# Performance work log

Measured on AMD Instinct MI355X. Metric: run time of the kernel, lower is better.

## Reference

```python
import jax, jax.numpy as jnp
import numpy as np

ALPHA = 0.2  # leaky relu slope
NEG_BIG = -9000000000000000.0


def setup_inputs() -> dict:
    key = jax.random.key(0)
    k1, k2, k3, k4 = jax.random.split(key, 4)
    B, N, Fin, Fout = 8, 2048, 256, 256
    h = jax.random.normal(k1, (B, N, Fin), dtype=jnp.float32)
    adj = jax.random.randint(k2, (B, N, N), 0, 2, dtype=jnp.int32)
    # xavier_uniform with gain=1.414
    gain = 1.414
    limW = gain * np.sqrt(6.0 / (Fin + Fout))
    W = jax.random.uniform(k3, (Fin, Fout), dtype=jnp.float32, minval=-limW, maxval=limW)
    lima = gain * np.sqrt(6.0 / (2 * Fout + 1))
    a = jax.random.uniform(k4, (2 * Fout, 1), dtype=jnp.float32, minval=-lima, maxval=lima)
    return {"h": h, "adj": adj, "W": W, "a": a}


def reference(h, adj, W, a):
    # Wh: [B, N, F]
    Wh = jnp.matmul(h, W)
    Fout = W.shape[1]
    a1 = a[:Fout, 0]   # scores for source node i (repeat_interleave side)
    a2 = a[Fout:, 0]   # scores for target node j (repeat side)
    # e[b,i,j] = leakyrelu(Wh[b,i]@a1 + Wh[b,j]@a2)  -- decomposed, no O(N^2 * 2F) tensor
    s1 = jnp.einsum('bnf,f->bn', Wh, a1)  # [B, N]
    s2 = jnp.einsum('bnf,f->bn', Wh, a2)  # [B, N]
    e = jax.nn.leaky_relu(s1[:, :, None] + s2[:, None, :], negative_slope=ALPHA)
    masked = jnp.where(adj > 0, e, jnp.full_like(e, NEG_BIG))
    attention = jax.nn.softmax(masked, axis=2)  # dropout=0 (eval mode)
    h_prime = jnp.matmul(attention, Wh)  # [B, N, F]
    return jax.nn.elu(h_prime)
```

## Files before the change

### kernel.cpp

```cpp
#include <hip/hip_runtime.h>

typedef __attribute__((ext_vector_type(8))) short bhalf8;
typedef __attribute__((ext_vector_type(4))) float floatx4;

#define ALPHA_LR 0.2f

__device__ __forceinline__ unsigned short f2bf(float f) {
  union { float f; unsigned int u; } v; v.f = f;
  unsigned int r = v.u + 0x7fffu + ((v.u >> 16) & 1u);
  return (unsigned short)(r >> 16);
}
__device__ __forceinline__ float bf2f(unsigned short u) {
  union { unsigned int u; float f; } v; v.u = ((unsigned int)u) << 16;
  return v.f;
}
__device__ __forceinline__ void gld16(const void* g, void* l) {
  __builtin_amdgcn_global_load_lds((const __attribute__((address_space(1))) unsigned int*)g,
                                   (__attribute__((address_space(3))) unsigned int*)l,
                                   16, 0, 0);
}

__global__ void k0w_split(const float* __restrict__ W,
                          unsigned short* __restrict__ WThi,
                          unsigned short* __restrict__ WTlo,
                          unsigned int* __restrict__ s2maxEnc) {
  __shared__ float s[16][17];
  const int tx = threadIdx.x, ty = threadIdx.y;
  if (blockIdx.x == 0 && blockIdx.y == 0 && ty == 0 && tx < 8) s2maxEnc[tx] = 0u;
  const int n0 = blockIdx.x * 16, k0 = blockIdx.y * 16;
  s[ty][tx] = W[(k0 + ty) * 256 + n0 + tx];
  __syncthreads();
  float v = s[tx][ty];
  const int k = k0 + tx, n = n0 + ty;
  unsigned short hi = f2bf(v);
  unsigned short lo = f2bf(v - bf2f(hi));
  const int idx = (k >> 5) * 8192 + n * 32 + (k & 31);
  WThi[idx] = hi;
  WTlo[idx] = lo;
}

__global__ __launch_bounds__(512, 2) void k1_mfma(const float* __restrict__ h,
                                                  const unsigned short* __restrict__ Bhi_g,
                                                  const unsigned short* __restrict__ Blo_g,
                                                  const float* __restrict__ a_g,
                                                  unsigned short* __restrict__ WhPack,
                                                  float* __restrict__ s1,
                                                  float* __restrict__ s2,
                                                  unsigned int* __restrict__ s2maxEnc) {
  __shared__ unsigned short Ah[64 * 264], Al[64 * 264];
  __shared__ unsigned short Bh[2][8192], Bl[2][8192];
  __shared__ float s1red[64], s2red[64];
  const int t = threadIdx.x;
  const long r0 = (long)blockIdx.x * 64;
  const int wave = t >> 6, lane = t & 63;

  if (t < 64) { s1red[t] = 0.f; s2red[t] = 0.f; }

#pragma unroll
  for (int rep = 0; rep < 2; rep++) {
    const int off = wave * 1024 + rep * 512;
    gld16(Bhi_g + off + lane * 8, &Bh[0][off]);
    gld16(Blo_g + off + lane * 8, &Bl[0][off]);
  }

#pragma unroll
  for (int q = 0; q < 8; q++) {
    int idx = q * 512 + t;
    int row = idx >> 6, c4 = idx & 63;
    float4 x = *(const float4*)(h + (r0 + row) * 256 + c4 * 4);
    float xs[4] = {x.x, x.y, x.z, x.w};
    unsigned short hs[4], ls[4];
#pragma unroll
    for (int qq = 0; qq < 4; qq++) {
      hs[qq] = f2bf(xs[qq]);
      ls[qq] = f2bf(xs[qq] - bf2f(hs[qq]));
    }
    *(ushort4*)&Ah[row * 264 + c4 * 4] = (ushort4){hs[0], hs[1], hs[2], hs[3]};
    *(ushort4*)&Al[row * 264 + c4 * 4] = (ushort4){ls[0], ls[1], ls[2], ls[3]};
  }
  __syncthreads();

  const int wm = wave >> 2, wn = wave & 3;
  const int lhi = lane >> 4, llo = lane & 15;

  floatx4 acc[2][4];
#pragma unroll
  for (int mt = 0; mt < 2; mt++)
#pragma unroll
    for (int nt = 0; nt < 4; nt++) acc[mt][nt] = (floatx4){0.f, 0.f, 0.f, 0.f};

  for (int ks = 0; ks < 8; ks++) {
    const int cur = ks & 1, nxt = cur ^ 1, ksn = (ks + 1) & 7;
#pragma unroll
    for (int rep = 0; rep < 2; rep++) {
      const int off = wave * 1024 + rep * 512;
      gld16(Bhi_g + ksn * 8192 + off + lane * 8, &Bh[nxt][off]);
      gld16(Blo_g + ksn * 8192 + off + lane * 8, &Bl[nxt][off]);
    }

    const int k0 = ks * 32;
    bhalf8 ah[2], al[2], bh[4], bl[4];
#pragma unroll
    for (int mt = 0; mt < 2; mt++) {
      int ro = (wm * 32 + mt * 16 + llo) * 264 + k0 + lhi * 8;
      ah[mt] = *(const bhalf8*)&Ah[ro];
      al[mt] = *(const bhalf8*)&Al[ro];
    }
#pragma unroll
    for (int nt = 0; nt < 4; nt++) {
      int ro = (wn * 64 + nt * 16 + llo) * 32 + lhi * 8;
      bh[nt] = *(const bhalf8*)&Bh[cur][ro];
      bl[nt] = *(const bhalf8*)&Bl[cur][ro];
    }
#pragma unroll
    for (int mt = 0; mt < 2; mt++)
#pragma unroll
      for (int nt = 0; nt < 4; nt++) {
        acc[mt][nt] = __builtin_amdgcn_mfma_f32_16x16x32_bf16(ah[mt], bh[nt], acc[mt][nt], 0, 0, 0);
        acc[mt][nt] = __builtin_amdgcn_mfma_f32_16x16x32_bf16(ah[mt], bl[nt], acc[mt][nt], 0, 0, 0);
        acc[mt][nt] = __builtin_amdgcn_mfma_f32_16x16x32_bf16(al[mt], bh[nt], acc[mt][nt], 0, 0, 0);
      }
    __syncthreads();
  }

  float a1v[4], a2v[4];
#pragma unroll
  for (int nt = 0; nt < 4; nt++) {
    int f = wn * 64 + nt * 16 + llo;
    a1v[nt] = a_g[f];
    a2v[nt] = a_g[256 + f];
  }

  const int b = (int)(r0 >> 11);
  const int jt_base = (int)((r0 & 2047) >> 5);

#pragma unroll
  for (int mt = 0; mt < 2; mt++) {
    float p1[4], p2[4];
#pragma unroll
    for (int reg = 0; reg < 4; reg++) {
      p1[reg] = acc[mt][0][reg] * a1v[0] + acc[mt][1][reg] * a1v[1] +
                acc[mt][2][reg] * a1v[2] + acc[mt][3][reg] * a1v[3];
      p2[reg] = acc[mt][0][reg] * a2v[0] + acc[mt][1][reg] * a2v[1] +
                acc[mt][2][reg] * a2v[2] + acc[mt][3][reg] * a2v[3];
    }
#pragma unroll
    for (int off = 1; off < 16; off <<= 1) {
#pragma unroll
      for (int reg = 0; reg < 4; reg++) {
        p1[reg] += __shfl_xor(p1[reg], off);
        p2[reg] += __shfl_xor(p2[reg], off);
      }
    }
    if (llo == 0) {
#pragma unroll
      for (int reg = 0; reg < 4; reg++) {
        int il = wm * 32 + mt * 16 + lhi * 4 + reg;
        atomicAdd(&s1red[il], p1[reg]);
        atomicAdd(&s2red[il], p2[reg]);
      }
    }
#pragma unroll
    for (int nt = 0; nt < 4; nt++) {
      int f = wn * 64 + nt * 16 + llo;
      int jt = jt_base + wm;
      ushort4 pk = (ushort4){f2bf(acc[mt][nt][0]), f2bf(acc[mt][nt][1]),
                             f2bf(acc[mt][nt][2]), f2bf(acc[mt][nt][3])};
      *(ushort4*)&WhPack[((long)((b * 64 + jt) * 256 + f)) * 32 + mt * 16 + lhi * 4] = pk;
    }
  }

  __syncthreads();
  if (t < 64) {
    s1[r0 + t] = s1red[t];
    s2[r0 + t] = s2red[t];
    float v = s2red[t];
#pragma unroll
    for (int o = 32; o; o >>= 1) v = fmaxf(v, __shfl_xor(v, o));
    if (t == 0) {
      unsigned int u = __float_as_uint(v);
      unsigned int key = (u & 0x80000000u) ? ~u : (u | 0x80000000u);
      atomicMax(s2maxEnc + b, key);
    }
  }
}

__global__ __launch_bounds__(512, 2) void k3_attn(const unsigned short* __restrict__ WhPack,
                                                  const int* __restrict__ adj,
                                                  const float* __restrict__ s1g,
                                                  const float* __restrict__ s2g,
                                                  const unsigned int* __restrict__ s2maxEnc,
                                                  float* __restrict__ out) {
  const int t = threadIdx.x;
  const int lin = blockIdx.x;
  const int b = lin & 7;
  const int ig = lin >> 3;
  const int wave = t >> 6, lane = t & 63;
  const int rg = wave >> 2, fg = wave & 3;
  const int i0 = ig * 64 + rg * 32;
  const long gr0 = (long)b * 2048 + i0;
  const int llo = lane & 15, lhi = lane >> 4;

  const unsigned int ek = s2maxEnc[b];
  const float s2max = (ek & 0x80000000u) ? __uint_as_float(ek & 0x7fffffffu)
                                         : __uint_as_float(~ek);
  float s1i[2], Mi[2];
#pragma unroll
  for (int mt = 0; mt < 2; mt++) {
    s1i[mt] = s1g[gr0 + mt * 16 + llo];
    float xm = s1i[mt] + s2max;
    Mi[mt] = fmaxf(xm, ALPHA_LR * xm);
  }

  const float* s2p = s2g + (long)b * 2048 + lhi * 8;
  const int* ap0 = adj + (gr0 + llo) * 2048 + lhi * 8;
  const int* ap1 = ap0 + 16 * 2048;
  const unsigned short* wb =
      WhPack + (long)b * 524288 + (long)((fg * 64 + llo) * 32 + lhi * 8);

  int4 cA0 = *(const int4*)ap0, cB0 = *(const int4*)(ap0 + 4);
  int4 cA1 = *(const int4*)ap1, cB1 = *(const int4*)(ap1 + 4);
  int4 nA0 = *(const int4*)(ap0 + 32), nB0 = *(const int4*)(ap0 + 36);
  int4 nA1 = *(const int4*)(ap1 + 32), nB1 = *(const int4*)(ap1 + 36);
  float4 s2A = *(const float4*)s2p;
  float4 s2B = *(const float4*)(s2p + 4);
  bhalf8 bF[4];
#pragma unroll
  for (int nt = 0; nt < 4; nt++) bF[nt] = *(const bhalf8*)(wb + nt * 512);

  floatx4 acc[2][4];
#pragma unroll
  for (int mt = 0; mt < 2; mt++)
#pragma unroll
    for (int nt = 0; nt < 4; nt++) acc[mt][nt] = (floatx4){0.f, 0.f, 0.f, 0.f};
  float ls0 = 0.f, ls1 = 0.f;

#pragma unroll 2
  for (int jt = 0; jt < 64; jt++) {
    const int jn = (jt < 63) ? jt + 1 : 63;
    const int j2 = (jt < 62) ? jt + 2 : 63;

    bhalf8 bFn[4];
#pragma unroll
    for (int nt = 0; nt < 4; nt++)
      bFn[nt] = *(const bhalf8*)(wb + (long)jn * 8192 + nt * 512);
    float4 s2nA = *(const float4*)(s2p + jn * 32);
    float4 s2nB = *(const float4*)(s2p + jn * 32 + 4);
    int4 mA0 = *(const int4*)(ap0 + j2 * 32), mB0 = *(const int4*)(ap0 + j2 * 32 + 4);
    int4 mA1 = *(const int4*)(ap1 + j2 * 32), mB1 = *(const int4*)(ap1 + j2 * 32 + 4);

    __builtin_amdgcn_sched_barrier(0);

    bhalf8 pa[2];
#pragma unroll
    for (int mt = 0; mt < 2; mt++) {
      const float s1v = s1i[mt], miv = Mi[mt];
      const int4 aA = mt ? cA1 : cA0;
      const int4 aB = mt ? cB1 : cB0;
      float xs[8] = {s2A.x, s2A.y, s2A.z, s2A.w, s2B.x, s2B.y, s2B.z, s2B.w};
      int am[8] = {aA.x, aA.y, aA.z, aA.w, aB.x, aB.y, aB.z, aB.w};
      float e[8];
      float lsm = 0.f;
#pragma unroll
      for (int q = 0; q < 8; q++) {
        float x = s1v + xs[q];
        float lk = fmaxf(x, ALPHA_LR * x);
        float ee = __expf(lk - miv);
        ee = (am[q] > 0) ? ee : 0.f;
        lsm += ee;
        e[q] = ee;
      }
      if (mt) ls1 += lsm; else ls0 += lsm;
      union { unsigned int u[4]; bhalf8 v; } pk;
#pragma unroll
      for (int q = 0; q < 4; q++)
        asm("v_cvt_pk_bf16_f32 %0, %1, %2" : "=v"(pk.u[q]) : "v"(e[2 * q]), "v"(e[2 * q + 1]));
      pa[mt] = pk.v;
    }

#pragma unroll
    for (int mt = 0; mt < 2; mt++)
#pragma unroll
      for (int nt = 0; nt < 4; nt++)
        acc[mt][nt] = __builtin_amdgcn_mfma_f32_16x16x32_bf16(mt ? pa[1] : pa[0],
                                                              bF[nt], acc[mt][nt], 0, 0, 0);

    cA0 = nA0; cB0 = nB0; cA1 = nA1; cB1 = nB1;
    nA0 = mA0; nB0 = mB0; nA1 = mA1; nB1 = mB1;
    s2A = s2nA; s2B = s2nB;
#pragma unroll
    for (int nt = 0; nt < 4; nt++) bF[nt] = bFn[nt];
  }

  ls0 += __shfl_xor(ls0, 16); ls0 += __shfl_xor(ls0, 32);
  ls1 += __shfl_xor(ls1, 16); ls1 += __shfl_xor(ls1, 32);
  float inv0 = 1.f / fmaxf(ls0, 1e-35f);
  float inv1 = 1.f / fmaxf(ls1, 1e-35f);

#pragma unroll
  for (int mt = 0; mt < 2; mt++) {
#pragma unroll
    for (int reg = 0; reg < 4; reg++) {
      const int rloc = lhi * 4 + reg;
      float iv = __shfl(mt ? inv1 : inv0, rloc);
      const long orow = (gr0 + mt * 16 + rloc) * 256 + fg * 64 + llo;
#pragma unroll
      for (int nt = 0; nt < 4; nt++) {
        float v = acc[mt][nt][reg] * iv;
        v = v > 0.f ? v : expm1f(v);
        out[orow + nt * 16] = v;
      }
    }
  }
}

extern "C" void kernel_launch(void* const* d_in, const int* in_sizes, int n_in,
                              void* d_out, int out_size, void* d_ws, size_t ws_size,
                              hipStream_t stream) {
  const float* h = (const float*)d_in[0];
  const int* adj = (const int*)d_in[1];
  const float* W = (const float*)d_in[2];
  const float* a = (const float*)d_in[3];
  float* out = (float*)d_out;

  char* ws = (char*)d_ws;
  unsigned short* WhPack = (unsigned short*)ws;
  unsigned short* WThi = (unsigned short*)(ws + 8388608);
  unsigned short* WTlo = (unsigned short*)(ws + 8519680);
  float* s1 = (float*)(ws + 8650752);
  float* s2 = (float*)(ws + 8716288);
  unsigned int* s2maxEnc = (unsigned int*)(ws + 8781824);

  hipLaunchKernelGGL(k0w_split, dim3(16, 16), dim3(16, 16), 0, stream, W, WThi, WTlo, s2maxEnc);
  hipLaunchKernelGGL(k1_mfma, dim3(256), dim3(512), 0, stream, h, WThi, WTlo, a,
                     WhPack, s1, s2, s2maxEnc);
  hipLaunchKernelGGL(k3_attn, dim3(256), dim3(512), 0, stream, WhPack, adj,
                     s1, s2, s2maxEnc, out);
}
```

Before: 288.8 us.

## Pack adjacency into bitmask in a pre-pass and read bits in attention kernel

Adds a streaming kernel that reads the int32 adjacency matrix once with coalesced loads and uses wave ballots to write a 1-bit-per-edge mask. The attention kernel then loads one 32-bit mask word per row per tile instead of eight int32 values per lane, and drops its two-tile-ahead adjacency prefetch. The aim is to shrink the attention kernel's memory traffic and register pressure, and to remove redundant adjacency reads across the feature-group waves. The cost is an extra kernel launch and a separate full pass over the 128MB adjacency tensor.

```diff
diff --git a/kernel.cpp b/kernel.cpp
--- a/kernel.cpp
+++ b/kernel.cpp
@@ -39,6 +39,31 @@
   WTlo[idx] = lo;
 }
 
+__global__ __launch_bounds__(256) void k2_pack(const int* __restrict__ adj,
+                                               unsigned long long* __restrict__ mask) {
+  const int wave = threadIdx.x >> 6, lane = threadIdx.x & 63;
+  const long wid = (long)blockIdx.x * 4 + wave;
+  const long u0 = wid * 64;
+  const int* base = adj + u0 * 64 + lane;
+#pragma unroll
+  for (int it = 0; it < 64; it += 4) {
+    int v0 = base[(it + 0) * 64];
+    int v1 = base[(it + 1) * 64];
+    int v2 = base[(it + 2) * 64];
+    int v3 = base[(it + 3) * 64];
+    unsigned long long m0 = __ballot(v0 > 0);
+    unsigned long long m1 = __ballot(v1 > 0);
+    unsigned long long m2 = __ballot(v2 > 0);
+    unsigned long long m3 = __ballot(v3 > 0);
+    if (lane == 0) {
+      mask[u0 + it + 0] = m0;
+      mask[u0 + it + 1] = m1;
+      mask[u0 + it + 2] = m2;
+      mask[u0 + it + 3] = m3;
+    }
+  }
+}
+
 __global__ __launch_bounds__(512, 2) void k1_mfma(const float* __restrict__ h,
                                                   const unsigned short* __restrict__ Bhi_g,
                                                   const unsigned short* __restrict__ Blo_g,
@@ -186,7 +211,7 @@
 }
 
 __global__ __launch_bounds__(512, 2) void k3_attn(const unsigned short* __restrict__ WhPack,
-                                                  const int* __restrict__ adj,
+                                                  const unsigned int* __restrict__ mask32,
                                                   const float* __restrict__ s1g,
                                                   const float* __restrict__ s2g,
                                                   const unsigned int* __restrict__ s2maxEnc,
@@ -200,6 +225,7 @@
   const int i0 = ig * 64 + rg * 32;
   const long gr0 = (long)b * 2048 + i0;
   const int llo = lane & 15, lhi = lane >> 4;
+  const int sh = lhi * 8;
 
   const unsigned int ek = s2maxEnc[b];
   const float s2max = (ek & 0x80000000u) ? __uint_as_float(ek & 0x7fffffffu)
@@ -213,15 +239,12 @@
   }
 
   const float* s2p = s2g + (long)b * 2048 + lhi * 8;
-  const int* ap0 = adj + (gr0 + llo) * 2048 + lhi * 8;
-  const int* ap1 = ap0 + 16 * 2048;
+  const unsigned int* mp0 = mask32 + (gr0 + llo) * 64;
+  const unsigned int* mp1 = mp0 + 16 * 64;
   const unsigned short* wb =
       WhPack + (long)b * 524288 + (long)((fg * 64 + llo) * 32 + lhi * 8);
 
-  int4 cA0 = *(const int4*)ap0, cB0 = *(const int4*)(ap0 + 4);
-  int4 cA1 = *(const int4*)ap1, cB1 = *(const int4*)(ap1 + 4);
-  int4 nA0 = *(const int4*)(ap0 + 32), nB0 = *(const int4*)(ap0 + 36);
-  int4 nA1 = *(const int4*)(ap1 + 32), nB1 = *(const int4*)(ap1 + 36);
+  unsigned int cm0 = mp0[0], cm1 = mp1[0];
   float4 s2A = *(const float4*)s2p;
   float4 s2B = *(const float4*)(s2p + 4);
   bhalf8 bF[4];
@@ -238,7 +261,6 @@
 #pragma unroll 2
   for (int jt = 0; jt < 64; jt++) {
     const int jn = (jt < 63) ? jt + 1 : 63;
-    const int j2 = (jt < 62) ? jt + 2 : 63;
 
     bhalf8 bFn[4];
 #pragma unroll
@@ -246,8 +268,7 @@
       bFn[nt] = *(const bhalf8*)(wb + (long)jn * 8192 + nt * 512);
     float4 s2nA = *(const float4*)(s2p + jn * 32);
     float4 s2nB = *(const float4*)(s2p + jn * 32 + 4);
-    int4 mA0 = *(const int4*)(ap0 + j2 * 32), mB0 = *(const int4*)(ap0 + j2 * 32 + 4);
-    int4 mA1 = *(const int4*)(ap1 + j2 * 32), mB1 = *(const int4*)(ap1 + j2 * 32 + 4);
+    unsigned int nm0 = mp0[jn], nm1 = mp1[jn];
 
     __builtin_amdgcn_sched_barrier(0);
 
@@ -255,10 +276,8 @@
 #pragma unroll
     for (int mt = 0; mt < 2; mt++) {
       const float s1v = s1i[mt], miv = Mi[mt];
-      const int4 aA = mt ? cA1 : cA0;
-      const int4 aB = mt ? cB1 : cB0;
+      const unsigned int mb = ((mt ? cm1 : cm0) >> sh) & 0xffu;
       float xs[8] = {s2A.x, s2A.y, s2A.z, s2A.w, s2B.x, s2B.y, s2B.z, s2B.w};
-      int am[8] = {aA.x, aA.y, aA.z, aA.w, aB.x, aB.y, aB.z, aB.w};
       float e[8];
       float lsm = 0.f;
 #pragma unroll
@@ -266,7 +285,7 @@
         float x = s1v + xs[q];
         float lk = fmaxf(x, ALPHA_LR * x);
         float ee = __expf(lk - miv);
-        ee = (am[q] > 0) ? ee : 0.f;
+        ee = (mb & (1u << q)) ? ee : 0.f;
         lsm += ee;
         e[q] = ee;
       }
@@ -285,8 +304,7 @@
         acc[mt][nt] = __builtin_amdgcn_mfma_f32_16x16x32_bf16(mt ? pa[1] : pa[0],
                                                               bF[nt], acc[mt][nt], 0, 0, 0);
 
-    cA0 = nA0; cB0 = nB0; cA1 = nA1; cB1 = nB1;
-    nA0 = mA0; nB0 = mB0; nA1 = mA1; nB1 = mB1;
+    cm0 = nm0; cm1 = nm1;
     s2A = s2nA; s2B = s2nB;
 #pragma unroll
     for (int nt = 0; nt < 4; nt++) bF[nt] = bFn[nt];
@@ -330,10 +348,12 @@
   float* s1 = (float*)(ws + 8650752);
   float* s2 = (float*)(ws + 8716288);
   unsigned int* s2maxEnc = (unsigned int*)(ws + 8781824);
+  unsigned long long* adjMask = (unsigned long long*)(ws + 8912896);
 
   hipLaunchKernelGGL(k0w_split, dim3(16, 16), dim3(16, 16), 0, stream, W, WThi, WTlo, s2maxEnc);
   hipLaunchKernelGGL(k1_mfma, dim3(256), dim3(512), 0, stream, h, WThi, WTlo, a,
                      WhPack, s1, s2, s2maxEnc);
-  hipLaunchKernelGGL(k3_attn, dim3(256), dim3(512), 0, stream, WhPack, adj,
-                     s1, s2, s2maxEnc, out);
-}
+  hipLaunchKernelGGL(k2_pack, dim3(2048), dim3(256), 0, stream, adj, adjMask);
+  hipLaunchKernelGGL(k3_attn, dim3(256), dim3(512), 0, stream, WhPack,
+                     (const unsigned int*)adjMask, s1, s2, s2maxEnc, out);
+}
```

Measured after the change: 297.1 us. 2.9% more time.
